# Kernel optimization log

Hardware: AMD Instinct MI355X
Metric: run time of the kernel (lower is better)

Reference implementation:

```python
import jax, jax.numpy as jnp
import numpy as np

D_MODEL = 1024
N_EXPERTS = 8
TOP_K = 2
LN_EPS = 1e-5


def setup_inputs() -> dict:
    key = jax.random.key(0)
    ks = jax.random.split(key, 8)
    B, S, d, E = 2, 2048, D_MODEL, N_EXPERTS
    f = 2 * d
    s_in = 0.02
    return {
        "x": jax.random.normal(ks[0], (B, S, d), jnp.float32),
        "Wg": jax.random.normal(ks[1], (d, E), jnp.float32) * s_in,
        "bg": jnp.zeros((E,), jnp.float32),
        "W1": jax.random.normal(ks[2], (E, d, f), jnp.float32) * s_in,
        "b1": jnp.zeros((E, f), jnp.float32),
        "W2": jax.random.normal(ks[3], (E, f, d), jnp.float32) * s_in,
        "b2": jnp.zeros((E, d), jnp.float32),
        "gamma": jnp.ones((d,), jnp.float32),
        "beta": jnp.zeros((d,), jnp.float32),
    }


def reference(x, Wg, bg, W1, b1, W2, b2, gamma, beta):
    # Gating + top-k routing (softmax over the selected top-k logits only)
    logits = jnp.einsum("bsd,de->bse", x, Wg) + bg            # [B,S,E]
    topk_vals, topk_idx = jax.lax.top_k(logits, TOP_K)         # [B,S,K]
    topk_w = jax.nn.softmax(topk_vals, axis=-1)                # [B,S,K]

    # Expert MLPs evaluated densely for all experts (dropout is identity in eval)
    h = jax.nn.relu(jnp.einsum("bsd,edf->bsef", x, W1) + b1)   # [B,S,E,2d]
    eo = jnp.einsum("bsef,efd->bsed", h, W2) + b2              # [B,S,E,d]

    # Gather the top-k experts' outputs per token and combine with gate weights
    sel = jnp.take_along_axis(eo, topk_idx[..., None], axis=2)  # [B,S,K,d]
    mixed = jnp.sum(sel * topk_w[..., None], axis=2)            # [B,S,d]

    # Residual + LayerNorm
    y = mixed + x
    mu = jnp.mean(y, axis=-1, keepdims=True)
    var = jnp.mean(jnp.square(y - mu), axis=-1, keepdims=True)
    return gamma * (y - mu) * jax.lax.rsqrt(var + LN_EPS) + beta
```

## Files before the change

### kernel.cpp

```cpp
#include <hip/hip_runtime.h>


typedef unsigned short ushort_t;
typedef short short8 __attribute__((ext_vector_type(8)));
typedef float f32x4 __attribute__((ext_vector_type(4)));

#define T_TOKENS 4096
#define DMODEL 1024
#define FFN 2048
#define NEXP 8
#define MAXSLOTS 9216
#define GATE_BLOCKS 256
#define TOK_PER_BLK 16
#define MAX_MT 12

__device__ __forceinline__ ushort_t f2bf(float f) {
    unsigned u = __float_as_uint(f);
    return (ushort_t)((u + 0x7fffu + ((u >> 16) & 1u)) >> 16);
}
__device__ __forceinline__ float bflo(unsigned packed) {
    return __uint_as_float(packed << 16);
}
__device__ __forceinline__ float bfhi(unsigned packed) {
    return __uint_as_float(packed & 0xffff0000u);
}

__device__ __forceinline__ void gload_lds16(const void* g, void* l) {
    __builtin_amdgcn_global_load_lds(
        (const __attribute__((address_space(1))) unsigned int*)g,
        (__attribute__((address_space(3))) unsigned int*)l,
        16, 0, 0);
}

__global__ __launch_bounds__(256) void gate_kernel(
    const float* __restrict__ x, const float* __restrict__ Wg,
    const float* __restrict__ bg,
    int* __restrict__ top_idx, float* __restrict__ top_w,
    int* __restrict__ blk_hist)
{
    __shared__ int hist[NEXP];
    const int tid = threadIdx.x, lane = tid & 63, w = tid >> 6;
    if (tid < NEXP) hist[tid] = 0;
    __syncthreads();

    float wreg[16][8];
    #pragma unroll
    for (int i = 0; i < 16; i++) {
        const float4* wp = (const float4*)&Wg[(i * 64 + lane) * 8];
        float4 a = wp[0], b = wp[1];
        wreg[i][0] = a.x; wreg[i][1] = a.y; wreg[i][2] = a.z; wreg[i][3] = a.w;
        wreg[i][4] = b.x; wreg[i][5] = b.y; wreg[i][6] = b.z; wreg[i][7] = b.w;
    }
    float bgv[8];
    #pragma unroll
    for (int e = 0; e < 8; e++) bgv[e] = bg[e];

    const int t0 = blockIdx.x * TOK_PER_BLK + w * 4;
    #pragma unroll 1
    for (int it = 0; it < 4; it++) {
        int t = t0 + it;
        const float* xr = x + (size_t)t * DMODEL;
        float acc[8] = {0.f,0.f,0.f,0.f,0.f,0.f,0.f,0.f};
        #pragma unroll
        for (int i = 0; i < 16; i++) {
            float xv = xr[i * 64 + lane];
            #pragma unroll
            for (int e = 0; e < 8; e++) acc[e] += xv * wreg[i][e];
        }
        #pragma unroll
        for (int off = 32; off > 0; off >>= 1) {
            #pragma unroll
            for (int e = 0; e < 8; e++) acc[e] += __shfl_down(acc[e], off);
        }
        if (lane == 0) {
            float l[8];
            #pragma unroll
            for (int e = 0; e < 8; e++) l[e] = acc[e] + bgv[e];
            int i0 = 0; float v0 = l[0];
            #pragma unroll
            for (int e = 1; e < 8; e++) if (l[e] > v0) { v0 = l[e]; i0 = e; }
            int i1 = -1; float v1 = -1e30f;
            #pragma unroll
            for (int e = 0; e < 8; e++) if (e != i0 && l[e] > v1) { v1 = l[e]; i1 = e; }
            float eg = expf(v1 - v0);
            float den = 1.f + eg;
            int p0 = atomicAdd(&hist[i0], 1);
            int p1 = atomicAdd(&hist[i1], 1);
            top_idx[2 * t]     = i0 | (p0 << 4);
            top_idx[2 * t + 1] = i1 | (p1 << 4);
            top_w[2 * t]     = 1.f / den;
            top_w[2 * t + 1] = eg / den;
        }
    }
    __syncthreads();
    if (tid < NEXP) blk_hist[blockIdx.x * NEXP + tid] = hist[tid];
}

__global__ __launch_bounds__(512) void scan_kernel(
    const int* __restrict__ blk_hist, int* __restrict__ blk_base,
    int* __restrict__ offs)
{
    __shared__ int cnt[NEXP];
    const int tid = threadIdx.x, lane = tid & 63, e = tid >> 6;
    int carry = 0;
    #pragma unroll
    for (int r = 0; r < GATE_BLOCKS / 64; r++) {
        int b = r * 64 + lane;
        int orig = blk_hist[b * NEXP + e];
        int v = orig;
        #pragma unroll
        for (int off = 1; off < 64; off <<= 1) {
            int u = __shfl_up(v, off);
            if (lane >= off) v += u;
        }
        blk_base[b * NEXP + e] = carry + v - orig;
        carry += __shfl(v, 63);
    }
    if (lane == 0) cnt[e] = carry;
    __syncthreads();
    if (tid == 0) {
        int cum = 0;
        for (int ee = 0; ee < NEXP; ee++) {
            offs[ee] = cum;
            cum += (cnt[ee] + 127) & ~127;
        }
        offs[NEXP] = cum;
    }
}

__global__ __launch_bounds__(256) void scatter_gather_kernel(
    const float* __restrict__ x, const int* __restrict__ top_idx,
    const int* __restrict__ offs, const int* __restrict__ blk_base,
    int* __restrict__ slot_of, ushort_t* __restrict__ Xg)
{
    const int t = blockIdx.x, tid = threadIdx.x;
    __shared__ int slots[2];
    if (tid < 2) {
        int v = top_idx[2 * t + tid];
        int e = v & 15, pos = v >> 4;
        int gb = t / TOK_PER_BLK;
        int slot = offs[e] + blk_base[gb * NEXP + e] + pos;
        slot_of[2 * t + tid] = slot;
        slots[tid] = slot;
    }
    __syncthreads();
    float4 xv = ((const float4*)(x + (size_t)t * DMODEL))[tid];
    uint2 pk;
    pk.x = f2bf(xv.x) | ((unsigned)f2bf(xv.y) << 16);
    pk.y = f2bf(xv.z) | ((unsigned)f2bf(xv.w) << 16);
    ((uint2*)(Xg + (size_t)slots[0] * DMODEL))[tid] = pk;
    ((uint2*)(Xg + (size_t)slots[1] * DMODEL))[tid] = pk;
}

__global__ __launch_bounds__(256) void transpose_kernel(
    const float* __restrict__ W1, const float* __restrict__ W2,
    ushort_t* __restrict__ W1T, ushort_t* __restrict__ W2T)
{
    int b = blockIdx.x;
    const float* s; ushort_t* d; int Rs, Cs, rt, ct;
    if (b < 4096) {
        int e = b >> 9, t = b & 511;
        rt = t >> 5; ct = t & 31;
        s = W1 + (size_t)e * DMODEL * FFN;
        d = W1T + (size_t)e * DMODEL * FFN;
        Rs = DMODEL; Cs = FFN;
    } else {
        b -= 4096;
        int e = b >> 9, t = b & 511;
        rt = t >> 4; ct = t & 15;
        s = W2 + (size_t)e * DMODEL * FFN;
        d = W2T + (size_t)e * DMODEL * FFN;
        Rs = FFN; Cs = DMODEL;
    }
    const int r0 = rt * 64, c0 = ct * 64;
    const int ty = threadIdx.x & 15, tx = threadIdx.x >> 4;

    float v[4][4];
    #pragma unroll
    for (int i = 0; i < 4; i++) {
        float4 ld = *(const float4*)&s[(size_t)(r0 + ty * 4 + i) * Cs + c0 + tx * 4];
        v[i][0] = ld.x; v[i][1] = ld.y; v[i][2] = ld.z; v[i][3] = ld.w;
    }
    #pragma unroll
    for (int j = 0; j < 4; j++) {
        uint2 pk;
        pk.x = f2bf(v[0][j]) | ((unsigned)f2bf(v[1][j]) << 16);
        pk.y = f2bf(v[2][j]) | ((unsigned)f2bf(v[3][j]) << 16);
        *(uint2*)&d[(size_t)(c0 + tx * 4 + j) * Rs + r0 + ty * 4] = pk;
    }
}

template <int K, int N, bool RELU>
__global__ __launch_bounds__(256) void expert_gemm(
    const ushort_t* __restrict__ A,
    const ushort_t* __restrict__ Bt,
    const float* __restrict__ bias,
    ushort_t* __restrict__ Cout,
    const int* __restrict__ offs)
{
    const int e  = blockIdx.x;
    const int nt = blockIdx.y;
    const int mt = blockIdx.z;
    const int off_e = offs[e];
    const int Mpad  = offs[e + 1] - off_e;
    if (mt * 128 >= Mpad) return;

    __shared__ __align__(16) ushort_t As[128 * 32];
    __shared__ __align__(16) ushort_t Bs[128 * 32];

    const int tid  = threadIdx.x;
    const int lane = tid & 63;
    const int w    = tid >> 6;
    const int quad = lane >> 4;
    const int r16  = lane & 15;
    const int lrow = lane >> 2;
    const int lk   = (((lane & 3) ^ ((lane >> 3) & 3))) * 8;

    const size_t arow0 = (size_t)(off_e + mt * 128);
    const ushort_t* aS0 = A + (arow0 + (size_t)(2 * w + 0) * 16 + lrow) * K + lk;
    const ushort_t* aS1 = A + (arow0 + (size_t)(2 * w + 1) * 16 + lrow) * K + lk;
    const ushort_t* Bte = Bt + (size_t)e * N * K;
    const ushort_t* bS0 = Bte + ((size_t)(nt * 128 + (2 * w + 0) * 16 + lrow)) * K + lk;
    const ushort_t* bS1 = Bte + ((size_t)(nt * 128 + (2 * w + 1) * 16 + lrow)) * K + lk;
    ushort_t* aD0 = &As[(2 * w + 0) * 512];
    ushort_t* aD1 = &As[(2 * w + 1) * 512];
    ushort_t* bD0 = &Bs[(2 * w + 0) * 512];
    ushort_t* bD1 = &Bs[(2 * w + 1) * 512];

    const int wm = (w >> 1) * 64;
    const int wn = (w & 1) * 64;
    const int sw = ((r16 >> 1) & 3) ^ quad;

    f32x4 acc[4][4];
    #pragma unroll
    for (int i = 0; i < 4; i++)
        #pragma unroll
        for (int j = 0; j < 4; j++)
            acc[i][j] = (f32x4){0.f, 0.f, 0.f, 0.f};

    for (int k0 = 0; k0 < K; k0 += 32) {
        gload_lds16(aS0 + k0, aD0);
        gload_lds16(aS1 + k0, aD1);
        gload_lds16(bS0 + k0, bD0);
        gload_lds16(bS1 + k0, bD1);
        __syncthreads();
        short8 af[4], bfr[4];
        #pragma unroll
        for (int i = 0; i < 4; i++)
            af[i] = *(const short8*)&As[(wm + i * 16 + r16) * 32 + sw * 8];
        #pragma unroll
        for (int j = 0; j < 4; j++)
            bfr[j] = *(const short8*)&Bs[(wn + j * 16 + r16) * 32 + sw * 8];
        #pragma unroll
        for (int i = 0; i < 4; i++)
            #pragma unroll
            for (int j = 0; j < 4; j++)
                acc[i][j] = __builtin_amdgcn_mfma_f32_16x16x32_bf16(
                    af[i], bfr[j], acc[i][j], 0, 0, 0);
        __syncthreads();
    }

    const float* be = bias + (size_t)e * N;
    #pragma unroll
    for (int i = 0; i < 4; i++) {
        #pragma unroll
        for (int j = 0; j < 4; j++) {
            int n = nt * 128 + wn + j * 16 + r16;
            float bv = be[n];
            #pragma unroll
            for (int r = 0; r < 4; r++) {
                int m = mt * 128 + wm + i * 16 + quad * 4 + r;
                float v = acc[i][j][r] + bv;
                if (RELU) v = v > 0.f ? v : 0.f;
                Cout[(size_t)(off_e + m) * N + n] = f2bf(v);
            }
        }
    }
}

__global__ __launch_bounds__(256) void ln_kernel(
    const float* __restrict__ x, const ushort_t* __restrict__ O,
    const int* __restrict__ slot_of, const float* __restrict__ top_w,
    const float* __restrict__ gamma, const float* __restrict__ beta,
    float* __restrict__ out)
{
    int t = blockIdx.x, tid = threadIdx.x;
    int s0 = slot_of[2 * t], s1 = slot_of[2 * t + 1];
    float w0 = top_w[2 * t], w1 = top_w[2 * t + 1];
    float4 xv = ((const float4*)(x + (size_t)t * DMODEL))[tid];
    uint2 a = ((const uint2*)(O + (size_t)s0 * DMODEL))[tid];
    uint2 b = ((const uint2*)(O + (size_t)s1 * DMODEL))[tid];

    float y[4];
    y[0] = xv.x + w0 * bflo(a.x) + w1 * bflo(b.x);
    y[1] = xv.y + w0 * bfhi(a.x) + w1 * bfhi(b.x);
    y[2] = xv.z + w0 * bflo(a.y) + w1 * bflo(b.y);
    y[3] = xv.w + w0 * bfhi(a.y) + w1 * bfhi(b.y);

    float s = y[0] + y[1] + y[2] + y[3];
    float sq = y[0]*y[0] + y[1]*y[1] + y[2]*y[2] + y[3]*y[3];
    __shared__ float red[2][4];
    #pragma unroll
    for (int off = 32; off > 0; off >>= 1) {
        s += __shfl_down(s, off);
        sq += __shfl_down(sq, off);
    }
    int lane = tid & 63, wv = tid >> 6;
    if (lane == 0) { red[0][wv] = s; red[1][wv] = sq; }
    __syncthreads();
    if (tid == 0) {
        float S = red[0][0] + red[0][1] + red[0][2] + red[0][3];
        float SQ = red[1][0] + red[1][1] + red[1][2] + red[1][3];
        float mu = S * (1.f / DMODEL);
        float var = SQ * (1.f / DMODEL) - mu * mu;
        red[0][0] = mu;
        red[1][0] = rsqrtf(var + 1e-5f);
    }
    __syncthreads();
    float mu = red[0][0], inv = red[1][0];
    float4 gv = ((const float4*)gamma)[tid];
    float4 bv = ((const float4*)beta)[tid];
    float4 ov;
    ov.x = gv.x * (y[0] - mu) * inv + bv.x;
    ov.y = gv.y * (y[1] - mu) * inv + bv.y;
    ov.z = gv.z * (y[2] - mu) * inv + bv.z;
    ov.w = gv.w * (y[3] - mu) * inv + bv.w;
    ((float4*)(out + (size_t)t * DMODEL))[tid] = ov;
}

extern "C" void kernel_launch(void* const* d_in, const int* in_sizes, int n_in,
                              void* d_out, int out_size, void* d_ws, size_t ws_size,
                              hipStream_t stream)
{
    const float* x     = (const float*)d_in[0];
    const float* Wg    = (const float*)d_in[1];
    const float* bg    = (const float*)d_in[2];
    const float* W1    = (const float*)d_in[3];
    const float* b1    = (const float*)d_in[4];
    const float* W2    = (const float*)d_in[5];
    const float* b2    = (const float*)d_in[6];
    const float* gamma = (const float*)d_in[7];
    const float* beta  = (const float*)d_in[8];
    float* out = (float*)d_out;

    char* ws = (char*)d_ws;
    size_t o = 0;
    auto alloc = [&](size_t bytes) {
        size_t r = o;
        o = (o + bytes + 255) & ~(size_t)255;
        return r;
    };
    size_t o_offs    = alloc((NEXP + 1) * 4);
    size_t o_topidx  = alloc((size_t)T_TOKENS * 2 * 4);
    size_t o_topw    = alloc((size_t)T_TOKENS * 2 * 4);
    size_t o_slotof  = alloc((size_t)T_TOKENS * 2 * 4);
    size_t o_bhist   = alloc((size_t)GATE_BLOCKS * NEXP * 4);
    size_t o_bbase   = alloc((size_t)GATE_BLOCKS * NEXP * 4);
    size_t o_w1t     = alloc((size_t)NEXP * DMODEL * FFN * 2);
    size_t o_w2t     = alloc((size_t)NEXP * DMODEL * FFN * 2);
    size_t o_xg      = alloc((size_t)MAXSLOTS * DMODEL * 2);
    size_t o_h       = alloc((size_t)MAXSLOTS * FFN * 2);
    size_t o_obuf    = alloc((size_t)MAXSLOTS * DMODEL * 2);
    (void)ws_size; (void)in_sizes; (void)n_in; (void)out_size;

    int*      offs     = (int*)(ws + o_offs);
    int*      top_idx  = (int*)(ws + o_topidx);
    float*    top_w    = (float*)(ws + o_topw);
    int*      slot_of  = (int*)(ws + o_slotof);
    int*      blk_hist = (int*)(ws + o_bhist);
    int*      blk_base = (int*)(ws + o_bbase);
    ushort_t* W1T      = (ushort_t*)(ws + o_w1t);
    ushort_t* W2T      = (ushort_t*)(ws + o_w2t);
    ushort_t* Xg       = (ushort_t*)(ws + o_xg);
    ushort_t* H        = (ushort_t*)(ws + o_h);
    ushort_t* Obuf     = (ushort_t*)(ws + o_obuf);

    gate_kernel<<<GATE_BLOCKS, 256, 0, stream>>>(x, Wg, bg, top_idx, top_w, blk_hist);
    transpose_kernel<<<8192, 256, 0, stream>>>(W1, W2, W1T, W2T);
    scan_kernel<<<1, 512, 0, stream>>>(blk_hist, blk_base, offs);
    scatter_gather_kernel<<<T_TOKENS, 256, 0, stream>>>(x, top_idx, offs, blk_base, slot_of, Xg);
    expert_gemm<DMODEL, FFN, true>
        <<<dim3(NEXP, FFN / 128, MAX_MT), 256, 0, stream>>>(Xg, W1T, b1, H, offs);
    expert_gemm<FFN, DMODEL, false>
        <<<dim3(NEXP, DMODEL / 128, MAX_MT), 256, 0, stream>>>(H, W2T, b2, Obuf, offs);
    ln_kernel<<<T_TOKENS, 256, 0, stream>>>(x, Obuf, slot_of, top_w, gamma, beta, out);
}
```

Baseline: 316.3 us.

## Stage weight transpose through LDS, widen gate grid, and prefetch scan inputs

The weight transpose-to-bf16 kernel now loads a 64x64 fp32 tile into padded shared memory and writes 16-byte contiguous bf16 stores per output row, replacing 8-byte strided stores. This is meant to improve write coalescing on the 16M-element weight conversion. The gate kernel now uses one token per wave across 1024 blocks instead of four tokens per wave across 256 blocks, giving more parallelism but reloading Wg per token. The scan kernel loads all per-block histograms up front before the shuffle scans.

```diff
diff --git a/kernel.cpp b/kernel.cpp
--- a/kernel.cpp
+++ b/kernel.cpp
@@ -10,8 +10,8 @@
 #define FFN 2048
 #define NEXP 8
 #define MAXSLOTS 9216
-#define GATE_BLOCKS 256
-#define TOK_PER_BLK 16
+#define GATE_BLOCKS 1024
+#define TOK_PER_BLK 4
 #define MAX_MT 12
 
 __device__ __forceinline__ ushort_t f2bf(float f) {
@@ -43,54 +43,42 @@
     if (tid < NEXP) hist[tid] = 0;
     __syncthreads();
 
-    float wreg[16][8];
+    const int t = blockIdx.x * TOK_PER_BLK + w;
+    const float* xr = x + (size_t)t * DMODEL;
+    float acc[8] = {0.f,0.f,0.f,0.f,0.f,0.f,0.f,0.f};
     #pragma unroll
     for (int i = 0; i < 16; i++) {
+        float xv = xr[i * 64 + lane];
         const float4* wp = (const float4*)&Wg[(i * 64 + lane) * 8];
         float4 a = wp[0], b = wp[1];
-        wreg[i][0] = a.x; wreg[i][1] = a.y; wreg[i][2] = a.z; wreg[i][3] = a.w;
-        wreg[i][4] = b.x; wreg[i][5] = b.y; wreg[i][6] = b.z; wreg[i][7] = b.w;
-    }
-    float bgv[8];
-    #pragma unroll
-    for (int e = 0; e < 8; e++) bgv[e] = bg[e];
-
-    const int t0 = blockIdx.x * TOK_PER_BLK + w * 4;
-    #pragma unroll 1
-    for (int it = 0; it < 4; it++) {
-        int t = t0 + it;
-        const float* xr = x + (size_t)t * DMODEL;
-        float acc[8] = {0.f,0.f,0.f,0.f,0.f,0.f,0.f,0.f};
-        #pragma unroll
-        for (int i = 0; i < 16; i++) {
-            float xv = xr[i * 64 + lane];
-            #pragma unroll
-            for (int e = 0; e < 8; e++) acc[e] += xv * wreg[i][e];
-        }
-        #pragma unroll
-        for (int off = 32; off > 0; off >>= 1) {
-            #pragma unroll
-            for (int e = 0; e < 8; e++) acc[e] += __shfl_down(acc[e], off);
-        }
-        if (lane == 0) {
-            float l[8];
-            #pragma unroll
-            for (int e = 0; e < 8; e++) l[e] = acc[e] + bgv[e];
-            int i0 = 0; float v0 = l[0];
-            #pragma unroll
-            for (int e = 1; e < 8; e++) if (l[e] > v0) { v0 = l[e]; i0 = e; }
-            int i1 = -1; float v1 = -1e30f;
-            #pragma unroll
-            for (int e = 0; e < 8; e++) if (e != i0 && l[e] > v1) { v1 = l[e]; i1 = e; }
-            float eg = expf(v1 - v0);
-            float den = 1.f + eg;
-            int p0 = atomicAdd(&hist[i0], 1);
-            int p1 = atomicAdd(&hist[i1], 1);
-            top_idx[2 * t]     = i0 | (p0 << 4);
-            top_idx[2 * t + 1] = i1 | (p1 << 4);
-            top_w[2 * t]     = 1.f / den;
-            top_w[2 * t + 1] = eg / den;
-        }
+        acc[0] += xv * a.x; acc[1] += xv * a.y;
+        acc[2] += xv * a.z; acc[3] += xv * a.w;
+        acc[4] += xv * b.x; acc[5] += xv * b.y;
+        acc[6] += xv * b.z; acc[7] += xv * b.w;
+    }
+    #pragma unroll
+    for (int off = 32; off > 0; off >>= 1) {
+        #pragma unroll
+        for (int e = 0; e < 8; e++) acc[e] += __shfl_down(acc[e], off);
+    }
+    if (lane == 0) {
+        float l[8];
+        #pragma unroll
+        for (int e = 0; e < 8; e++) l[e] = acc[e] + bg[e];
+        int i0 = 0; float v0 = l[0];
+        #pragma unroll
+        for (int e = 1; e < 8; e++) if (l[e] > v0) { v0 = l[e]; i0 = e; }
+        int i1 = -1; float v1 = -1e30f;
+        #pragma unroll
+        for (int e = 0; e < 8; e++) if (e != i0 && l[e] > v1) { v1 = l[e]; i1 = e; }
+        float eg = expf(v1 - v0);
+        float den = 1.f + eg;
+        int p0 = atomicAdd(&hist[i0], 1);
+        int p1 = atomicAdd(&hist[i1], 1);
+        top_idx[2 * t]     = i0 | (p0 << 4);
+        top_idx[2 * t + 1] = i1 | (p1 << 4);
+        top_w[2 * t]     = 1.f / den;
+        top_w[2 * t + 1] = eg / den;
     }
     __syncthreads();
     if (tid < NEXP) blk_hist[blockIdx.x * NEXP + tid] = hist[tid];
@@ -102,18 +90,20 @@
 {
     __shared__ int cnt[NEXP];
     const int tid = threadIdx.x, lane = tid & 63, e = tid >> 6;
+    int orig[GATE_BLOCKS / 64];
+    #pragma unroll
+    for (int r = 0; r < GATE_BLOCKS / 64; r++)
+        orig[r] = blk_hist[(r * 64 + lane) * NEXP + e];
     int carry = 0;
     #pragma unroll
     for (int r = 0; r < GATE_BLOCKS / 64; r++) {
-        int b = r * 64 + lane;
-        int orig = blk_hist[b * NEXP + e];
-        int v = orig;
+        int v = orig[r];
         #pragma unroll
         for (int off = 1; off < 64; off <<= 1) {
             int u = __shfl_up(v, off);
             if (lane >= off) v += u;
         }
-        blk_base[b * NEXP + e] = carry + v - orig;
+        blk_base[(r * 64 + lane) * NEXP + e] = carry + v - orig[r];
         carry += __shfl(v, 63);
     }
     if (lane == 0) cnt[e] = carry;
@@ -173,20 +163,45 @@
         Rs = FFN; Cs = DMODEL;
     }
     const int r0 = rt * 64, c0 = ct * 64;
-    const int ty = threadIdx.x & 15, tx = threadIdx.x >> 4;
-
-    float v[4][4];
-    #pragma unroll
-    for (int i = 0; i < 4; i++) {
-        float4 ld = *(const float4*)&s[(size_t)(r0 + ty * 4 + i) * Cs + c0 + tx * 4];
-        v[i][0] = ld.x; v[i][1] = ld.y; v[i][2] = ld.z; v[i][3] = ld.w;
-    }
-    #pragma unroll
-    for (int j = 0; j < 4; j++) {
-        uint2 pk;
-        pk.x = f2bf(v[0][j]) | ((unsigned)f2bf(v[1][j]) << 16);
-        pk.y = f2bf(v[2][j]) | ((unsigned)f2bf(v[3][j]) << 16);
-        *(uint2*)&d[(size_t)(c0 + tx * 4 + j) * Rs + r0 + ty * 4] = pk;
+    const int tid = threadIdx.x;
+
+    __shared__ float tile[64][65];
+
+    {
+        const int r  = tid >> 4;
+        const int c4 = (tid & 15) * 4;
+        #pragma unroll
+        for (int p = 0; p < 4; p++) {
+            float4 v = *(const float4*)&s[(size_t)(r0 + p * 16 + r) * Cs + c0 + c4];
+            tile[p * 16 + r][c4 + 0] = v.x;
+            tile[p * 16 + r][c4 + 1] = v.y;
+            tile[p * 16 + r][c4 + 2] = v.z;
+            tile[p * 16 + r][c4 + 3] = v.w;
+        }
+    }
+    __syncthreads();
+
+    {
+        const int c  = tid >> 2;
+        const int rb = (tid & 3) * 8;
+        uint4 o0, o1;
+        {
+            unsigned p0 = (unsigned)f2bf(tile[rb + 0][c]) | ((unsigned)f2bf(tile[rb + 1][c]) << 16);
+            unsigned p1 = (unsigned)f2bf(tile[rb + 2][c]) | ((unsigned)f2bf(tile[rb + 3][c]) << 16);
+            unsigned p2 = (unsigned)f2bf(tile[rb + 4][c]) | ((unsigned)f2bf(tile[rb + 5][c]) << 16);
+            unsigned p3 = (unsigned)f2bf(tile[rb + 6][c]) | ((unsigned)f2bf(tile[rb + 7][c]) << 16);
+            o0.x = p0; o0.y = p1; o0.z = p2; o0.w = p3;
+        }
+        {
+            unsigned p0 = (unsigned)f2bf(tile[rb + 32][c]) | ((unsigned)f2bf(tile[rb + 33][c]) << 16);
+            unsigned p1 = (unsigned)f2bf(tile[rb + 34][c]) | ((unsigned)f2bf(tile[rb + 35][c]) << 16);
+            unsigned p2 = (unsigned)f2bf(tile[rb + 36][c]) | ((unsigned)f2bf(tile[rb + 37][c]) << 16);
+            unsigned p3 = (unsigned)f2bf(tile[rb + 38][c]) | ((unsigned)f2bf(tile[rb + 39][c]) << 16);
+            o1.x = p0; o1.y = p1; o1.z = p2; o1.w = p3;
+        }
+        ushort_t* drow = d + (size_t)(c0 + c) * Rs + r0;
+        *(uint4*)&drow[rb]      = o0;
+        *(uint4*)&drow[rb + 32] = o1;
     }
 }
 
```

Result: no change. 319.6 us (+1.0%).
